# Performance work log

Hardware: AMD Instinct MI355X
Metric: run time of the kernel (lower is better)

The kernel has to match this reference:

```python
import jax, jax.numpy as jnp
import numpy as np
from jax import lax

IN_CH = 256
NF = 128
B, H, W = 8, 256, 256


def _bn_relu(y, s, b):
    # inference-mode BatchNorm folded into per-channel affine, then ReLU
    return jax.nn.relu(y * s[None, :, None, None] + b[None, :, None, None])


def _upsample_bilinear_ac(x, scale):
    # bilinear upsample, align_corners=True (matches torch nn.Upsample)
    b, c, h, w = x.shape
    Ho, Wo = h * scale, w * scale
    ys = jnp.arange(Ho, dtype=x.dtype) * ((h - 1) / (Ho - 1))
    xs = jnp.arange(Wo, dtype=x.dtype) * ((w - 1) / (Wo - 1))
    y0 = jnp.floor(ys).astype(jnp.int32)
    x0 = jnp.floor(xs).astype(jnp.int32)
    y1 = jnp.minimum(y0 + 1, h - 1)
    x1 = jnp.minimum(x0 + 1, w - 1)
    wy = (ys - y0.astype(x.dtype))[None, None, :, None]
    wx = (xs - x0.astype(x.dtype))[None, None, None, :]
    # interpolate rows then columns
    top = x[:, :, y0, :] * (1 - wy) + x[:, :, y1, :] * wy      # [b,c,Ho,w]
    out = top[:, :, :, x0] * (1 - wx) + top[:, :, :, x1] * wx  # [b,c,Ho,Wo]
    return out


def setup_inputs() -> dict:
    key = jax.random.key(0)
    ks = jax.random.split(key, 6)
    inp = {
        "x": jax.random.normal(ks[0], (B, 64, H, W), dtype=jnp.float32),
        "w1": jax.random.normal(ks[1], (IN_CH, 64, 8, 8), dtype=jnp.float32) * 0.02,
        "bn1_s": jnp.ones((IN_CH,), jnp.float32),
        "bn1_b": jnp.zeros((IN_CH,), jnp.float32),
        "w_fai": jax.random.normal(ks[2], (NF, IN_CH), dtype=jnp.float32) * 0.05,
        "bnf_s": jnp.ones((NF,), jnp.float32),
        "bnf_b": jnp.zeros((NF,), jnp.float32),
        "w_sit": jax.random.normal(ks[3], (NF, IN_CH), dtype=jnp.float32) * 0.05,
        "bns_s": jnp.ones((NF,), jnp.float32),
        "bns_b": jnp.zeros((NF,), jnp.float32),
        "w_gama": jax.random.normal(ks[4], (NF, IN_CH), dtype=jnp.float32) * 0.05,
        "bng_s": jnp.ones((NF,), jnp.float32),
        "bng_b": jnp.zeros((NF,), jnp.float32),
    }
    return inp


def reference(x, w1, bn1_s, bn1_b, w_fai, bnf_s, bnf_b, w_sit, bns_s, bns_b,
              w_gama, bng_s, bng_b):
    # conv1: 8x8 stride-8 conv, BN, ReLU  -> [B, IN_CH, h, w]
    y = lax.conv_general_dilated(x, w1, window_strides=(8, 8), padding="VALID",
                                 dimension_numbers=("NCHW", "OIHW", "NCHW"))
    y = _bn_relu(y, bn1_s, bn1_b)
    b, c, h, w = y.shape
    n = h * w
    # 1x1 conv projections (einsum), BN, ReLU
    fai = _bn_relu(jnp.einsum("bchw,oc->bohw", y, w_fai), bnf_s, bnf_b)
    sit = _bn_relu(jnp.einsum("bchw,oc->bohw", y, w_sit), bns_s, bns_b)
    gama = _bn_relu(jnp.einsum("bchw,oc->bohw", y, w_gama), bng_s, bng_b)
    fai = fai.reshape(b, NF, n)
    sit = sit.reshape(b, NF, n)
    gama = gama.reshape(b, NF, n)
    # non-local attention: sigmoid(fai^T sit) @ gama^T
    sf = jax.nn.sigmoid(jnp.einsum("bcn,bcm->bnm", fai, sit))  # [b, n, n]
    out = jnp.einsum("bnm,bcm->bcn", sf, gama)                  # [b, NF, n]
    out = out.reshape(b, NF, h, w)
    return _upsample_bilinear_ac(out, 8)
```

## Files before the change

kernel.cpp:

```cpp
#include <hip/hip_runtime.h>

typedef __attribute__((ext_vector_type(8))) short short8_t;
typedef __attribute__((ext_vector_type(4))) float float4_t;

__device__ __forceinline__ unsigned short f2bf(float f) {
    unsigned int u = __float_as_uint(f);
    return (unsigned short)((u + 0x7FFFu + ((u >> 16) & 1u)) >> 16);
}
__device__ __forceinline__ unsigned int pkbf(float a, float b) {
    return (unsigned int)f2bf(a) | ((unsigned int)f2bf(b) << 16);
}

__global__ __launch_bounds__(512, 2) void k_conv1(
    const float* __restrict__ x, const float* __restrict__ w1,
    float* __restrict__ part)
{
    __shared__ unsigned short At[128 * 40];
    __shared__ unsigned short Bt[256 * 40];
    const int tid = threadIdx.x;
    const int mt = blockIdx.x, kc = blockIdx.y;
    const int m0 = mt * 128;
    const int bi = mt >> 3;
    const int oh0 = (mt & 7) * 4;
    const int lane = tid & 63, wid = tid >> 6;
    const int wm = wid & 1, wn = wid >> 1;
    const int quad = lane >> 4, r16 = lane & 15;
    const bool isA = tid < 256;
    const int tA = tid & 255;
    const int rA = tA >> 4, segA = tA & 15;
    const int ohl = rA >> 2, khl = rA & 3;
    const int rowA = ohl * 32 + segA * 2;
    const int koffA = (khl ^ (segA & 3)) * 8;
    const int kbase = kc * 1024;
    float4_t acc[4][4] = {};
    float4 ra[4];
    float4 rb[8];

    if (isA) {
        const int ic = kbase >> 6, kh0 = (kbase >> 3) & 7;
        const int xr = (oh0 + ohl) * 8 + kh0 + khl;
        const float4* s4 = (const float4*)(x + (((bi * 64 + ic) * 256 + xr) * 256 + segA * 16));
        ra[0] = s4[0]; ra[1] = s4[1]; ra[2] = s4[2]; ra[3] = s4[3];
    } else {
        #pragma unroll
        for (int l = 0; l < 8; ++l) {
            const int slot = l * 256 + tA;
            const int row = slot >> 3, p = slot & 7;
            rb[l] = *(const float4*)(w1 + row * 4096 + kbase + p * 4);
        }
    }

    for (int it = 0; it < 32; ++it) {
        if (isA) {
            int4 p0, p1;
            p0.x = pkbf(ra[0].x, ra[0].y); p0.y = pkbf(ra[0].z, ra[0].w);
            p0.z = pkbf(ra[1].x, ra[1].y); p0.w = pkbf(ra[1].z, ra[1].w);
            p1.x = pkbf(ra[2].x, ra[2].y); p1.y = pkbf(ra[2].z, ra[2].w);
            p1.z = pkbf(ra[3].x, ra[3].y); p1.w = pkbf(ra[3].z, ra[3].w);
            *(int4*)&At[rowA * 40 + koffA] = p0;
            *(int4*)&At[(rowA + 1) * 40 + koffA] = p1;
        } else {
            #pragma unroll
            for (int l = 0; l < 8; ++l) {
                const int slot = l * 256 + tA;
                const int row = slot >> 3, p = slot & 7;
                int2 wv; wv.x = pkbf(rb[l].x, rb[l].y); wv.y = pkbf(rb[l].z, rb[l].w);
                *(int2*)&Bt[row * 40 + p * 4] = wv;
            }
        }
        __syncthreads();
        if (it + 1 < 32) {
            const int k0 = kbase + (it + 1) * 32;
            if (isA) {
                const int ic = k0 >> 6, kh0 = (k0 >> 3) & 7;
                const int xr = (oh0 + ohl) * 8 + kh0 + khl;
                const float4* s4 = (const float4*)(x + (((bi * 64 + ic) * 256 + xr) * 256 + segA * 16));
                ra[0] = s4[0]; ra[1] = s4[1]; ra[2] = s4[2]; ra[3] = s4[3];
            } else {
                #pragma unroll
                for (int l = 0; l < 8; ++l) {
                    const int slot = l * 256 + tA;
                    const int row = slot >> 3, p = slot & 7;
                    rb[l] = *(const float4*)(w1 + row * 4096 + k0 + p * 4);
                }
            }
        }
        short8_t aF[4], bF[4];
        #pragma unroll
        for (int i = 0; i < 4; ++i) {
            const int R = wm * 64 + i * 16 + r16;
            aF[i] = *(const short8_t*)&At[R * 40 + (quad ^ ((r16 >> 1) & 3)) * 8];
        }
        #pragma unroll
        for (int j = 0; j < 4; ++j)
            bF[j] = *(const short8_t*)&Bt[(wn * 64 + j * 16 + r16) * 40 + quad * 8];
        #pragma unroll
        for (int i = 0; i < 4; ++i)
            #pragma unroll
            for (int j = 0; j < 4; ++j)
                acc[i][j] = __builtin_amdgcn_mfma_f32_16x16x32_bf16(aF[i], bF[j], acc[i][j], 0, 0, 0);
        __syncthreads();
    }
    float* pp = part + ((size_t)kc << 21);
    #pragma unroll
    for (int i = 0; i < 4; ++i) {
        const int mg = m0 + wm * 64 + i * 16 + quad * 4;
        #pragma unroll
        for (int j = 0; j < 4; ++j) {
            const int ng = wn * 64 + j * 16 + r16;
            #pragma unroll
            for (int r = 0; r < 4; ++r)
                pp[(mg + r) * 256 + ng] = acc[i][j][r];
        }
    }
}

__global__ __launch_bounds__(256, 4) void k_reduce(
    const float* __restrict__ part, const float* __restrict__ s1,
    const float* __restrict__ b1, unsigned short* __restrict__ y)
{
    const int id = blockIdx.x * 256 + threadIdx.x;
    const int c4 = id & 63;
    const float4* p = (const float4*)part + id;
    float4 a = p[0], b = p[524288], c = p[1048576], d = p[1572864];
    float4 s = ((const float4*)s1)[c4], bb = ((const float4*)b1)[c4];
    float vx = fmaxf((a.x + b.x + c.x + d.x) * s.x + bb.x, 0.f);
    float vy = fmaxf((a.y + b.y + c.y + d.y) * s.y + bb.y, 0.f);
    float vz = fmaxf((a.z + b.z + c.z + d.z) * s.z + bb.z, 0.f);
    float vw = fmaxf((a.w + b.w + c.w + d.w) * s.w + bb.w, 0.f);
    int2 o; o.x = pkbf(vx, vy); o.y = pkbf(vz, vw);
    ((int2*)y)[id] = o;
}

__global__ __launch_bounds__(256, 2) void k_proj3(
    const unsigned short* __restrict__ y,
    const float* __restrict__ w_fai, const float* __restrict__ w_sit,
    const float* __restrict__ w_gama,
    const float* __restrict__ fs, const float* __restrict__ fb,
    const float* __restrict__ ss, const float* __restrict__ sb,
    const float* __restrict__ gs, const float* __restrict__ gb,
    unsigned short* __restrict__ P, unsigned short* __restrict__ G)
{
    __shared__ unsigned short At[64 * 40];
    __shared__ unsigned short Bt[64 * 40];
    const int tid = threadIdx.x;
    const int nt = blockIdx.x, mt = blockIdx.y;
    const int m0 = mt * 64;
    const float *W, *S, *Bb;
    if (nt < 2)      { W = w_fai;  S = fs; Bb = fb; }
    else if (nt < 4) { W = w_sit;  S = ss; Bb = sb; }
    else             { W = w_gama; S = gs; Bb = gb; }
    const int roff = (nt * 64) & 127;
    const int lane = tid & 63, wid = tid >> 6;
    const int wm = wid & 1, wn = wid >> 1;
    const int quad = lane >> 4, r16 = lane & 15;
    float4_t acc[2][2] = {};

    for (int k0 = 0; k0 < 256; k0 += 32) {
        {
            const int row = tid >> 2, pp = tid & 3;
            *(int4*)&At[row * 40 + pp * 8] =
                *(const int4*)(y + (m0 + row) * 256 + k0 + pp * 8);
        }
        #pragma unroll
        for (int l = 0; l < 2; ++l) {
            const int slot = l * 256 + tid;
            const int row = slot >> 3, pp = slot & 7;
            float4 v = *(const float4*)(W + (roff + row) * 256 + k0 + pp * 4);
            int2 wv; wv.x = pkbf(v.x, v.y); wv.y = pkbf(v.z, v.w);
            *(int2*)&Bt[row * 40 + pp * 4] = wv;
        }
        __syncthreads();
        short8_t aF[2], bF[2];
        #pragma unroll
        for (int i = 0; i < 2; ++i)
            aF[i] = *(const short8_t*)&At[(wm * 32 + i * 16 + r16) * 40 + quad * 8];
        #pragma unroll
        for (int j = 0; j < 2; ++j)
            bF[j] = *(const short8_t*)&Bt[(wn * 32 + j * 16 + r16) * 40 + quad * 8];
        #pragma unroll
        for (int i = 0; i < 2; ++i)
            #pragma unroll
            for (int j = 0; j < 2; ++j)
                acc[i][j] = __builtin_amdgcn_mfma_f32_16x16x32_bf16(aF[i], bF[j], acc[i][j], 0, 0, 0);
        __syncthreads();
    }
    #pragma unroll
    for (int i = 0; i < 2; ++i) {
        const int mg = m0 + wm * 32 + i * 16 + quad * 4;
        #pragma unroll
        for (int j = 0; j < 2; ++j) {
            const int nl = wn * 32 + j * 16 + r16;
            const float sc = S[roff + nl], bc = Bb[roff + nl];
            if (nt < 4) {
                const int col = nt * 64 + nl;
                #pragma unroll
                for (int r = 0; r < 4; ++r) {
                    float v = fmaxf(acc[i][j][r] * sc + bc, 0.f);
                    P[(mg + r) * 256 + col] = f2bf(v);
                }
            } else {
                const int c = roff + nl;
                #pragma unroll
                for (int r = 0; r < 4; ++r) {
                    float v = fmaxf(acc[i][j][r] * sc + bc, 0.f);
                    const int sp = mg + r;
                    G[((sp >> 10) * 128 + c) * 1024 + (sp & 1023)] = f2bf(v);
                }
            }
        }
    }
}

__global__ __launch_bounds__(256, 2) void k_logits(
    const unsigned short* __restrict__ P, unsigned short* __restrict__ sf)
{
    __shared__ unsigned short At[128 * 40];
    __shared__ unsigned short Bt[64 * 40];
    const int tid = threadIdx.x;
    const int nt = blockIdx.x, mt = blockIdx.y, b = blockIdx.z;
    const int m0 = mt * 128, n0 = nt * 64;
    const int base = b * 1024;
    const int lane = tid & 63, wid = tid >> 6;
    const int wm = wid & 1, wn = wid >> 1;
    const int quad = lane >> 4, r16 = lane & 15;
    float4_t acc[4][2] = {};

    for (int k0 = 0; k0 < 128; k0 += 32) {
        #pragma unroll
        for (int j = 0; j < 2; ++j) {
            const int id = j * 256 + tid;
            const int row = id >> 2, p = id & 3;
            *(int4*)&At[row * 40 + p * 8] =
                *(const int4*)(P + (base + m0 + row) * 256 + k0 + p * 8);
        }
        {
            const int row = tid >> 2, p = tid & 3;
            *(int4*)&Bt[row * 40 + p * 8] =
                *(const int4*)(P + (base + n0 + row) * 256 + 128 + k0 + p * 8);
        }
        __syncthreads();
        short8_t aF[4], bF[2];
        #pragma unroll
        for (int i = 0; i < 4; ++i)
            aF[i] = *(const short8_t*)&At[(wm * 64 + i * 16 + r16) * 40 + quad * 8];
        #pragma unroll
        for (int j = 0; j < 2; ++j)
            bF[j] = *(const short8_t*)&Bt[(wn * 32 + j * 16 + r16) * 40 + quad * 8];
        #pragma unroll
        for (int i = 0; i < 4; ++i)
            #pragma unroll
            for (int j = 0; j < 2; ++j)
                acc[i][j] = __builtin_amdgcn_mfma_f32_16x16x32_bf16(aF[i], bF[j], acc[i][j], 0, 0, 0);
        __syncthreads();
    }
    #pragma unroll
    for (int i = 0; i < 4; ++i) {
        const int mg = m0 + wm * 64 + i * 16 + quad * 4;
        #pragma unroll
        for (int j = 0; j < 2; ++j) {
            const int ng = n0 + wn * 32 + j * 16 + r16;
            #pragma unroll
            for (int r = 0; r < 4; ++r) {
                float v = 1.0f / (1.0f + expf(-acc[i][j][r]));
                sf[b * 1048576 + (mg + r) * 1024 + ng] = f2bf(v);
            }
        }
    }
}

__global__ __launch_bounds__(256, 2) void k_av(
    const unsigned short* __restrict__ sf, const unsigned short* __restrict__ G,
    float* __restrict__ Opart)
{
    __shared__ unsigned short At[64 * 40];
    __shared__ unsigned short Bt[128 * 40];
    const int tid = threadIdx.x;
    const int mt = blockIdx.x, zz = blockIdx.y;
    const int b = zz >> 2, kc = zz & 3;
    const int m0 = mt * 64;
    const int lane = tid & 63, wid = tid >> 6;
    const int wm = wid & 1, wn = wid >> 1;
    const int quad = lane >> 4, r16 = lane & 15;
    float4_t acc[2][4] = {};

    for (int it = 0; it < 8; ++it) {
        const int k0 = kc * 256 + it * 32;
        {
            const int row = tid >> 2, p = tid & 3;
            *(int4*)&At[row * 40 + p * 8] =
                *(const int4*)(sf + b * 1048576 + (m0 + row) * 1024 + k0 + p * 8);
        }
        #pragma unroll
        for (int l = 0; l < 2; ++l) {
            const int slot = l * 256 + tid;
            const int row = slot >> 2, p = slot & 3;
            *(int4*)&Bt[row * 40 + p * 8] =
                *(const int4*)(G + (b * 128 + row) * 1024 + k0 + p * 8);
        }
        __syncthreads();
        short8_t aF[2], bF[4];
        #pragma unroll
        for (int i = 0; i < 2; ++i)
            aF[i] = *(const short8_t*)&At[(wm * 32 + i * 16 + r16) * 40 + quad * 8];
        #pragma unroll
        for (int j = 0; j < 4; ++j)
            bF[j] = *(const short8_t*)&Bt[(wn * 64 + j * 16 + r16) * 40 + quad * 8];
        #pragma unroll
        for (int i = 0; i < 2; ++i)
            #pragma unroll
            for (int j = 0; j < 4; ++j)
                acc[i][j] = __builtin_amdgcn_mfma_f32_16x16x32_bf16(aF[i], bF[j], acc[i][j], 0, 0, 0);
        __syncthreads();
    }
    float* op = Opart + (size_t)kc * 1048576 + (size_t)b * 131072;
    #pragma unroll
    for (int i = 0; i < 2; ++i) {
        const int mg = m0 + wm * 32 + i * 16 + quad * 4;
        #pragma unroll
        for (int j = 0; j < 4; ++j) {
            const int ng = wn * 64 + j * 16 + r16;
            #pragma unroll
            for (int r = 0; r < 4; ++r)
                op[(mg + r) * 128 + ng] = acc[i][j][r];
        }
    }
}

__global__ __launch_bounds__(256, 2) void k_up(
    const float* __restrict__ Opart, float* __restrict__ out)
{
    __shared__ float l0[32 * 136];
    __shared__ float l1[32 * 136];
    const int tid = threadIdx.x;
    const int yb = blockIdx.x, b = blockIdx.y;
    const float sc = 31.0f / 255.0f;
    const float fy = yb * sc;
    const int y0 = (int)fy;
    const float wy = fy - (float)y0;
    const int y1 = (y0 + 1 < 32) ? y0 + 1 : 31;
    const float4* r0 = (const float4*)(Opart + (size_t)b * 131072 + y0 * 4096);
    const float4* r1 = (const float4*)(Opart + (size_t)b * 131072 + y1 * 4096);
    #pragma unroll
    for (int j = 0; j < 4; ++j) {
        const int id = j * 256 + tid;
        const int xs = id >> 5, c4 = id & 31;
        float4 a0 = r0[id], a1 = r1[id];
        #pragma unroll
        for (int kc = 1; kc < 4; ++kc) {
            float4 t0 = r0[id + kc * 262144], t1 = r1[id + kc * 262144];
            a0.x += t0.x; a0.y += t0.y; a0.z += t0.z; a0.w += t0.w;
            a1.x += t1.x; a1.y += t1.y; a1.z += t1.z; a1.w += t1.w;
        }
        *(float4*)(l0 + xs * 136 + c4 * 4) = a0;
        *(float4*)(l1 + xs * 136 + c4 * 4) = a1;
    }
    __syncthreads();
    const float fx = tid * sc;
    const int x0 = (int)fx;
    const float wx = fx - (float)x0;
    const int x1 = (x0 + 1 < 32) ? x0 + 1 : 31;
    const float w00 = (1.f - wy) * (1.f - wx), w01 = (1.f - wy) * wx;
    const float w10 = wy * (1.f - wx), w11 = wy * wx;
    const float* a = l0 + x0 * 136;
    const float* bq = l0 + x1 * 136;
    const float* c = l1 + x0 * 136;
    const float* d = l1 + x1 * 136;
    float* op = out + (size_t)b * 8388608 + yb * 256 + tid;
    #pragma unroll 4
    for (int ch = 0; ch < 128; ++ch)
        op[ch * 65536] = w00 * a[ch] + w01 * bq[ch] + w10 * c[ch] + w11 * d[ch];
}

extern "C" void kernel_launch(void* const* d_in, const int* in_sizes, int n_in,
                              void* d_out, int out_size, void* d_ws, size_t ws_size,
                              hipStream_t stream) {
    (void)in_sizes; (void)n_in; (void)out_size; (void)ws_size;
    const float* x      = (const float*)d_in[0];
    const float* w1     = (const float*)d_in[1];
    const float* bn1_s  = (const float*)d_in[2];
    const float* bn1_b  = (const float*)d_in[3];
    const float* w_fai  = (const float*)d_in[4];
    const float* bnf_s  = (const float*)d_in[5];
    const float* bnf_b  = (const float*)d_in[6];
    const float* w_sit  = (const float*)d_in[7];
    const float* bns_s  = (const float*)d_in[8];
    const float* bns_b  = (const float*)d_in[9];
    const float* w_gama = (const float*)d_in[10];
    const float* bng_s  = (const float*)d_in[11];
    const float* bng_b  = (const float*)d_in[12];
    float* out = (float*)d_out;

    char* ws = (char*)d_ws;
    float*          pc    = (float*)ws;
    unsigned short* sf    = (unsigned short*)ws;
    float*          Opart = (float*)(ws + 16u * 1024 * 1024);
    unsigned short* y     = (unsigned short*)(ws + 32u * 1024 * 1024);
    unsigned short* P     = (unsigned short*)(ws + 36u * 1024 * 1024);
    unsigned short* G     = (unsigned short*)(ws + 40u * 1024 * 1024);

    k_conv1 <<<dim3(64, 4),    512, 0, stream>>>(x, w1, pc);
    k_reduce<<<dim3(2048),     256, 0, stream>>>(pc, bn1_s, bn1_b, y);
    k_proj3 <<<dim3(6, 128),   256, 0, stream>>>(y, w_fai, w_sit, w_gama,
                                                 bnf_s, bnf_b, bns_s, bns_b,
                                                 bng_s, bng_b, P, G);
    k_logits<<<dim3(16, 8, 8), 256, 0, stream>>>(P, sf);
    k_av    <<<dim3(16, 32),   256, 0, stream>>>(sf, G, Opart);
    k_up    <<<dim3(256, 8),   256, 0, stream>>>(Opart, out);
}
```

Baseline: 491.4 us.

## Fuse attention logits and AV kernels, pre-convert conv weights to bf16

Merges the logits+sigmoid kernel and the attention-times-values kernel into one k_attn kernel. The sigmoid tile now stays in LDS instead of writing and re-reading a 16 MB bf16 score matrix through global memory, and it uses fast exp/rcp. It also adds a small prep kernel that converts w1 to bf16 once per call. k_conv1 is reshaped to 256-thread blocks with a 64-row M tile, all threads loading both A and B, and B loaded directly as bf16. The tradeoff is more LDS per attention block, a recomputed-style split over key chunks, and one extra kernel launch.

```diff
diff --git a/kernel.cpp b/kernel.cpp
--- a/kernel.cpp
+++ b/kernel.cpp
@@ -11,84 +11,86 @@
     return (unsigned int)f2bf(a) | ((unsigned int)f2bf(b) << 16);
 }
 
-__global__ __launch_bounds__(512, 2) void k_conv1(
-    const float* __restrict__ x, const float* __restrict__ w1,
+__global__ __launch_bounds__(256) void k_wprep(
+    const float* __restrict__ w1, unsigned short* __restrict__ w1s)
+{
+    const int id = blockIdx.x * 256 + threadIdx.x;
+    const float4* s = (const float4*)(w1 + id * 8);
+    float4 a = s[0], b = s[1];
+    int4 o;
+    o.x = pkbf(a.x, a.y); o.y = pkbf(a.z, a.w);
+    o.z = pkbf(b.x, b.y); o.w = pkbf(b.z, b.w);
+    *(int4*)(w1s + id * 8) = o;
+}
+
+__global__ __launch_bounds__(256, 2) void k_conv1(
+    const float* __restrict__ x, const unsigned short* __restrict__ w1s,
     float* __restrict__ part)
 {
-    __shared__ unsigned short At[128 * 40];
+    __shared__ unsigned short At[64 * 40];
     __shared__ unsigned short Bt[256 * 40];
     const int tid = threadIdx.x;
     const int mt = blockIdx.x, kc = blockIdx.y;
-    const int m0 = mt * 128;
-    const int bi = mt >> 3;
-    const int oh0 = (mt & 7) * 4;
+    const int m0 = mt * 64;
+    const int bi = mt >> 4;
+    const int oh0 = (mt & 15) * 2;
     const int lane = tid & 63, wid = tid >> 6;
-    const int wm = wid & 1, wn = wid >> 1;
+    const int wn = wid;
     const int quad = lane >> 4, r16 = lane & 15;
-    const bool isA = tid < 256;
-    const int tA = tid & 255;
-    const int rA = tA >> 4, segA = tA & 15;
-    const int ohl = rA >> 2, khl = rA & 3;
-    const int rowA = ohl * 32 + segA * 2;
-    const int koffA = (khl ^ (segA & 3)) * 8;
+    const int ow  = tid & 31;
+    const int khl = (tid >> 5) & 3;
+    const int ohl = tid >> 7;
+    const int rowA  = ohl * 32 + ow;
+    const int koffA = (khl ^ ((rowA >> 1) & 3)) * 8;
     const int kbase = kc * 1024;
     float4_t acc[4][4] = {};
-    float4 ra[4];
-    float4 rb[8];
-
-    if (isA) {
-        const int ic = kbase >> 6, kh0 = (kbase >> 3) & 7;
+    float4 ra0, ra1;
+    int4 rb[4];
+
+    {
+        const int k0 = kbase;
+        const int ic = k0 >> 6, kh0 = (k0 >> 3) & 7;
         const int xr = (oh0 + ohl) * 8 + kh0 + khl;
-        const float4* s4 = (const float4*)(x + (((bi * 64 + ic) * 256 + xr) * 256 + segA * 16));
-        ra[0] = s4[0]; ra[1] = s4[1]; ra[2] = s4[2]; ra[3] = s4[3];
-    } else {
-        #pragma unroll
-        for (int l = 0; l < 8; ++l) {
-            const int slot = l * 256 + tA;
-            const int row = slot >> 3, p = slot & 7;
-            rb[l] = *(const float4*)(w1 + row * 4096 + kbase + p * 4);
-        }
-    }
-
+        const float4* s4 = (const float4*)(x + (((bi * 64 + ic) * 256 + xr) * 256 + ow * 8));
+        ra0 = s4[0]; ra1 = s4[1];
+        #pragma unroll
+        for (int l = 0; l < 4; ++l) {
+            const int slot = l * 256 + tid;
+            const int row = slot >> 2, p = slot & 3;
+            rb[l] = *(const int4*)(w1s + row * 4096 + k0 + p * 8);
+        }
+    }
     for (int it = 0; it < 32; ++it) {
-        if (isA) {
-            int4 p0, p1;
-            p0.x = pkbf(ra[0].x, ra[0].y); p0.y = pkbf(ra[0].z, ra[0].w);
-            p0.z = pkbf(ra[1].x, ra[1].y); p0.w = pkbf(ra[1].z, ra[1].w);
-            p1.x = pkbf(ra[2].x, ra[2].y); p1.y = pkbf(ra[2].z, ra[2].w);
-            p1.z = pkbf(ra[3].x, ra[3].y); p1.w = pkbf(ra[3].z, ra[3].w);
-            *(int4*)&At[rowA * 40 + koffA] = p0;
-            *(int4*)&At[(rowA + 1) * 40 + koffA] = p1;
-        } else {
-            #pragma unroll
-            for (int l = 0; l < 8; ++l) {
-                const int slot = l * 256 + tA;
-                const int row = slot >> 3, p = slot & 7;
-                int2 wv; wv.x = pkbf(rb[l].x, rb[l].y); wv.y = pkbf(rb[l].z, rb[l].w);
-                *(int2*)&Bt[row * 40 + p * 4] = wv;
+        {
+            int4 pa;
+            pa.x = pkbf(ra0.x, ra0.y); pa.y = pkbf(ra0.z, ra0.w);
+            pa.z = pkbf(ra1.x, ra1.y); pa.w = pkbf(ra1.z, ra1.w);
+            *(int4*)&At[rowA * 40 + koffA] = pa;
+            #pragma unroll
+            for (int l = 0; l < 4; ++l) {
+                const int slot = l * 256 + tid;
+                const int row = slot >> 2, p = slot & 3;
+                *(int4*)&Bt[row * 40 + p * 8] = rb[l];
             }
         }
         __syncthreads();
         if (it + 1 < 32) {
             const int k0 = kbase + (it + 1) * 32;
-            if (isA) {
-                const int ic = k0 >> 6, kh0 = (k0 >> 3) & 7;
-                const int xr = (oh0 + ohl) * 8 + kh0 + khl;
-                const float4* s4 = (const float4*)(x + (((bi * 64 + ic) * 256 + xr) * 256 + segA * 16));
-                ra[0] = s4[0]; ra[1] = s4[1]; ra[2] = s4[2]; ra[3] = s4[3];
-            } else {
-                #pragma unroll
-                for (int l = 0; l < 8; ++l) {
-                    const int slot = l * 256 + tA;
-                    const int row = slot >> 3, p = slot & 7;
-                    rb[l] = *(const float4*)(w1 + row * 4096 + k0 + p * 4);
-                }
+            const int ic = k0 >> 6, kh0 = (k0 >> 3) & 7;
+            const int xr = (oh0 + ohl) * 8 + kh0 + khl;
+            const float4* s4 = (const float4*)(x + (((bi * 64 + ic) * 256 + xr) * 256 + ow * 8));
+            ra0 = s4[0]; ra1 = s4[1];
+            #pragma unroll
+            for (int l = 0; l < 4; ++l) {
+                const int slot = l * 256 + tid;
+                const int row = slot >> 2, p = slot & 3;
+                rb[l] = *(const int4*)(w1s + row * 4096 + k0 + p * 8);
             }
         }
         short8_t aF[4], bF[4];
         #pragma unroll
         for (int i = 0; i < 4; ++i) {
-            const int R = wm * 64 + i * 16 + r16;
+            const int R = i * 16 + r16;
             aF[i] = *(const short8_t*)&At[R * 40 + (quad ^ ((r16 >> 1) & 3)) * 8];
         }
         #pragma unroll
@@ -104,7 +106,7 @@
     float* pp = part + ((size_t)kc << 21);
     #pragma unroll
     for (int i = 0; i < 4; ++i) {
-        const int mg = m0 + wm * 64 + i * 16 + quad * 4;
+        const int mg = m0 + i * 16 + quad * 4;
         #pragma unroll
         for (int j = 0; j < 4; ++j) {
             const int ng = wn * 64 + j * 16 + r16;
@@ -212,117 +214,108 @@
     }
 }
 
-__global__ __launch_bounds__(256, 2) void k_logits(
-    const unsigned short* __restrict__ P, unsigned short* __restrict__ sf)
-{
-    __shared__ unsigned short At[128 * 40];
-    __shared__ unsigned short Bt[64 * 40];
+#define LSTR 152
+__global__ __launch_bounds__(256, 2) void k_attn(
+    const unsigned short* __restrict__ P, const unsigned short* __restrict__ G,
+    float* __restrict__ Opart)
+{
+    __shared__ unsigned short At[64 * LSTR];
+    __shared__ unsigned short Bt[128 * LSTR];
+    __shared__ unsigned short Sl[64 * LSTR];
     const int tid = threadIdx.x;
-    const int nt = blockIdx.x, mt = blockIdx.y, b = blockIdx.z;
-    const int m0 = mt * 128, n0 = nt * 64;
+    const int nt = blockIdx.x, zz = blockIdx.y;
+    const int b = zz >> 2, kc = zz & 3;
+    const int n0 = nt * 64;
     const int base = b * 1024;
     const int lane = tid & 63, wid = tid >> 6;
     const int wm = wid & 1, wn = wid >> 1;
     const int quad = lane >> 4, r16 = lane & 15;
-    float4_t acc[4][2] = {};
-
-    for (int k0 = 0; k0 < 128; k0 += 32) {
-        #pragma unroll
-        for (int j = 0; j < 2; ++j) {
-            const int id = j * 256 + tid;
-            const int row = id >> 2, p = id & 3;
-            *(int4*)&At[row * 40 + p * 8] =
-                *(const int4*)(P + (base + m0 + row) * 256 + k0 + p * 8);
-        }
-        {
-            const int row = tid >> 2, p = tid & 3;
-            *(int4*)&Bt[row * 40 + p * 8] =
-                *(const int4*)(P + (base + n0 + row) * 256 + 128 + k0 + p * 8);
-        }
-        __syncthreads();
-        short8_t aF[4], bF[2];
-        #pragma unroll
-        for (int i = 0; i < 4; ++i)
-            aF[i] = *(const short8_t*)&At[(wm * 64 + i * 16 + r16) * 40 + quad * 8];
-        #pragma unroll
-        for (int j = 0; j < 2; ++j)
-            bF[j] = *(const short8_t*)&Bt[(wn * 32 + j * 16 + r16) * 40 + quad * 8];
-        #pragma unroll
-        for (int i = 0; i < 4; ++i)
-            #pragma unroll
-            for (int j = 0; j < 2; ++j)
-                acc[i][j] = __builtin_amdgcn_mfma_f32_16x16x32_bf16(aF[i], bF[j], acc[i][j], 0, 0, 0);
-        __syncthreads();
-    }
+    float4_t acc2[2][4] = {};
+
     #pragma unroll
-    for (int i = 0; i < 4; ++i) {
-        const int mg = m0 + wm * 64 + i * 16 + quad * 4;
-        #pragma unroll
-        for (int j = 0; j < 2; ++j) {
-            const int ng = n0 + wn * 32 + j * 16 + r16;
-            #pragma unroll
-            for (int r = 0; r < 4; ++r) {
-                float v = 1.0f / (1.0f + expf(-acc[i][j][r]));
-                sf[b * 1048576 + (mg + r) * 1024 + ng] = f2bf(v);
+    for (int l = 0; l < 4; ++l) {
+        const int slot = l * 256 + tid;
+        const int row = slot >> 4, p = slot & 15;
+        *(int4*)&At[row * LSTR + p * 8] =
+            *(const int4*)(P + (base + n0 + row) * 256 + p * 8);
+    }
+    for (int ms = 0; ms < 2; ++ms) {
+        const int m1 = kc * 256 + ms * 128;
+        #pragma unroll
+        for (int l = 0; l < 8; ++l) {
+            const int slot = l * 256 + tid;
+            const int row = slot >> 4, p = slot & 15;
+            *(int4*)&Bt[row * LSTR + p * 8] =
+                *(const int4*)(P + (base + m1 + row) * 256 + 128 + p * 8);
+        }
+        __syncthreads();
+        float4_t acc1[2][4] = {};
+        #pragma unroll
+        for (int c = 0; c < 4; ++c) {
+            short8_t aF[2], bF[4];
+            #pragma unroll
+            for (int i = 0; i < 2; ++i)
+                aF[i] = *(const short8_t*)&At[(wm * 32 + i * 16 + r16) * LSTR + c * 32 + quad * 8];
+            #pragma unroll
+            for (int j = 0; j < 4; ++j)
+                bF[j] = *(const short8_t*)&Bt[(wn * 64 + j * 16 + r16) * LSTR + c * 32 + quad * 8];
+            #pragma unroll
+            for (int i = 0; i < 2; ++i)
+                #pragma unroll
+                for (int j = 0; j < 4; ++j)
+                    acc1[i][j] = __builtin_amdgcn_mfma_f32_16x16x32_bf16(aF[i], bF[j], acc1[i][j], 0, 0, 0);
+        }
+        __syncthreads();
+        #pragma unroll
+        for (int i = 0; i < 2; ++i) {
+            const int nl = wm * 32 + i * 16 + quad * 4;
+            #pragma unroll
+            for (int j = 0; j < 4; ++j) {
+                const int ml = wn * 64 + j * 16 + r16;
+                #pragma unroll
+                for (int r = 0; r < 4; ++r) {
+                    const float xv = acc1[i][j][r];
+                    const float e = __expf(-xv);
+                    const float v = __builtin_amdgcn_rcpf(1.0f + e);
+                    Sl[(nl + r) * LSTR + ml] = f2bf(v);
+                }
             }
         }
-    }
-}
-
-__global__ __launch_bounds__(256, 2) void k_av(
-    const unsigned short* __restrict__ sf, const unsigned short* __restrict__ G,
-    float* __restrict__ Opart)
-{
-    __shared__ unsigned short At[64 * 40];
-    __shared__ unsigned short Bt[128 * 40];
-    const int tid = threadIdx.x;
-    const int mt = blockIdx.x, zz = blockIdx.y;
-    const int b = zz >> 2, kc = zz & 3;
-    const int m0 = mt * 64;
-    const int lane = tid & 63, wid = tid >> 6;
-    const int wm = wid & 1, wn = wid >> 1;
-    const int quad = lane >> 4, r16 = lane & 15;
-    float4_t acc[2][4] = {};
-
-    for (int it = 0; it < 8; ++it) {
-        const int k0 = kc * 256 + it * 32;
-        {
-            const int row = tid >> 2, p = tid & 3;
-            *(int4*)&At[row * 40 + p * 8] =
-                *(const int4*)(sf + b * 1048576 + (m0 + row) * 1024 + k0 + p * 8);
-        }
-        #pragma unroll
-        for (int l = 0; l < 2; ++l) {
+        #pragma unroll
+        for (int l = 0; l < 8; ++l) {
             const int slot = l * 256 + tid;
-            const int row = slot >> 2, p = slot & 3;
-            *(int4*)&Bt[row * 40 + p * 8] =
-                *(const int4*)(G + (b * 128 + row) * 1024 + k0 + p * 8);
-        }
-        __syncthreads();
-        short8_t aF[2], bF[4];
-        #pragma unroll
-        for (int i = 0; i < 2; ++i)
-            aF[i] = *(const short8_t*)&At[(wm * 32 + i * 16 + r16) * 40 + quad * 8];
-        #pragma unroll
-        for (int j = 0; j < 4; ++j)
-            bF[j] = *(const short8_t*)&Bt[(wn * 64 + j * 16 + r16) * 40 + quad * 8];
-        #pragma unroll
-        for (int i = 0; i < 2; ++i)
+            const int row = slot >> 4, p = slot & 15;
+            *(int4*)&Bt[row * LSTR + p * 8] =
+                *(const int4*)(G + (b * 128 + row) * 1024 + m1 + p * 8);
+        }
+        __syncthreads();
+        #pragma unroll
+        for (int c = 0; c < 4; ++c) {
+            short8_t aF[2], bF[4];
+            #pragma unroll
+            for (int i = 0; i < 2; ++i)
+                aF[i] = *(const short8_t*)&Sl[(wm * 32 + i * 16 + r16) * LSTR + c * 32 + quad * 8];
             #pragma unroll
             for (int j = 0; j < 4; ++j)
-                acc[i][j] = __builtin_amdgcn_mfma_f32_16x16x32_bf16(aF[i], bF[j], acc[i][j], 0, 0, 0);
+                bF[j] = *(const short8_t*)&Bt[(wn * 64 + j * 16 + r16) * LSTR + c * 32 + quad * 8];
+            #pragma unroll
+            for (int i = 0; i < 2; ++i)
+                #pragma unroll
+                for (int j = 0; j < 4; ++j)
+                    acc2[i][j] = __builtin_amdgcn_mfma_f32_16x16x32_bf16(aF[i], bF[j], acc2[i][j], 0, 0, 0);
+        }
         __syncthreads();
     }
     float* op = Opart + (size_t)kc * 1048576 + (size_t)b * 131072;
     #pragma unroll
     for (int i = 0; i < 2; ++i) {
-        const int mg = m0 + wm * 32 + i * 16 + quad * 4;
+        const int nl = n0 + wm * 32 + i * 16 + quad * 4;
         #pragma unroll
         for (int j = 0; j < 4; ++j) {
-            const int ng = wn * 64 + j * 16 + r16;
+            const int ch = wn * 64 + j * 16 + r16;
             #pragma unroll
             for (int r = 0; r < 4; ++r)
-                op[(mg + r) * 128 + ng] = acc[i][j][r];
+                op[(nl + r) * 128 + ch] = acc2[i][j][r];
         }
     }
 }
@@ -393,18 +386,18 @@
 
     char* ws = (char*)d_ws;
     float*          pc    = (float*)ws;
-    unsigned short* sf    = (unsigned short*)ws;
     float*          Opart = (float*)(ws + 16u * 1024 * 1024);
     unsigned short* y     = (unsigned short*)(ws + 32u * 1024 * 1024);
     unsigned short* P     = (unsigned short*)(ws + 36u * 1024 * 1024);
     unsigned short* G     = (unsigned short*)(ws + 40u * 1024 * 1024);
-
-    k_conv1 <<<dim3(64, 4),    512, 0, stream>>>(x, w1, pc);
+    unsigned short* w1s   = (unsigned short*)(ws + 44u * 1024 * 1024);
+
+    k_wprep <<<dim3(512),      256, 0, stream>>>(w1, w1s);
+    k_conv1 <<<dim3(128, 4),   256, 0, stream>>>(x, w1s, pc);
     k_reduce<<<dim3(2048),     256, 0, stream>>>(pc, bn1_s, bn1_b, y);
     k_proj3 <<<dim3(6, 128),   256, 0, stream>>>(y, w_fai, w_sit, w_gama,
                                                  bnf_s, bnf_b, bns_s, bns_b,
                                                  bng_s, bng_b, P, G);
-    k_logits<<<dim3(16, 8, 8), 256, 0, stream>>>(P, sf);
-    k_av    <<<dim3(16, 32),   256, 0, stream>>>(sf, G, Opart);
+    k_attn  <<<dim3(16, 32),   256, 0, stream>>>(P, G, Opart);
     k_up    <<<dim3(256, 8),   256, 0, stream>>>(Opart, out);
 }
```

Measured after the change: 510.1 us. +3.8%, slower.
